# Kernel tuning notes

Hardware: AMD Instinct MI355X
Metric: run time of the kernel (lower is better)

Reference implementation:

```python
import math
import jax
import jax.numpy as jnp
import numpy as np
from jax import lax

B, L, D = 4, 1024, 512
NL = 2           # encoder layers
E, K = 8, 4      # num_experts, top_k (SparseMoE defaults)
H = 4 * D        # expert hidden
NOISE_KEY = jax.random.key(42)


def _layer_norm(x, g, b, eps=1e-5):
    m = jnp.mean(x, axis=-1, keepdims=True)
    v = jnp.mean((x - m) ** 2, axis=-1, keepdims=True)
    return (x - m) * lax.rsqrt(v + eps) * g + b


def setup_inputs() -> dict:
    key = jax.random.key(0)
    ks = iter(jax.random.split(key, 64))
    s = 0.02

    def nrm(shape):
        return jax.random.normal(next(ks), shape, dtype=jnp.float32) * s

    inp = {
        "x": jax.random.normal(next(ks), (B, L, D), dtype=jnp.float32),
        "norm_coord": jax.random.uniform(next(ks), (B, L, 2), dtype=jnp.float32),
        "mask": jnp.triu(jnp.ones((L, L), dtype=bool), k=1),           # causal
        "src_key_padding_mask": jnp.zeros((B, L), dtype=bool),
        # per-layer stacked params (leading dim NL)
        "wq": nrm((NL, D, D)), "bq": jnp.zeros((NL, D)),
        "wk": nrm((NL, D, D)), "bk": jnp.zeros((NL, D)),
        "wv": nrm((NL, D, D)), "bv": jnp.zeros((NL, D)),
        "wr": nrm((NL, 2, D // 2)),                                    # RoPE freq proj (no bias)
        "ln1_g": jnp.ones((NL, D)), "ln1_b": jnp.zeros((NL, D)),
        "rt_w": nrm((NL, D, E)), "rt_b": jnp.zeros((NL, E)),           # router
        "nz_w": nrm((NL, D, E)), "nz_b": jnp.zeros((NL, E)),           # noise
        "ew1": nrm((NL, E, D, H)), "eb1": jnp.zeros((NL, E, H)),
        "ew2": nrm((NL, E, H, D)), "eb2": jnp.zeros((NL, E, D)),
        "ln2_g": jnp.ones((NL, D)), "ln2_b": jnp.zeros((NL, D)),
    }
    return inp


def _encoder(x, norm_coord, mask, src_key_padding_mask,
             wq, bq, wk, bk, wv, bv, wr, ln1_g, ln1_b,
             rt_w, rt_b, nz_w, nz_b, ew1, eb1, ew2, eb2, ln2_g, ln2_b):
    neg = jnp.float32(-jnp.inf)
    attn_mask = mask[None, :, :] | src_key_padding_mask[:, None, :]  # [B,L,L]
    for l in range(NL):
        # ---- RoPE attention ----
        q = x @ wq[l] + bq[l]
        k = x @ wk[l] + bk[l]
        v = x @ wv[l] + bv[l]
        f = norm_coord @ wr[l]                    # [B,L,D/2] angles
        cosf, sinf = jnp.cos(f), jnp.sin(f)

        def rot(t):
            t2 = t.reshape(B, L, D // 2, 2)
            re = t2[..., 0] * cosf - t2[..., 1] * sinf
            im = t2[..., 0] * sinf + t2[..., 1] * cosf
            return jnp.stack([re, im], axis=-1).reshape(B, L, D)

        q, k = rot(q), rot(k)
        scores = jnp.einsum("bqd,bkd->bqk", q, k) / math.sqrt(D)
        scores = jnp.where(attn_mask, neg, scores)
        attn = jax.nn.softmax(scores, axis=-1)
        x = x + jnp.einsum("bqk,bkd->bqd", attn, v)
        x = _layer_norm(x, ln1_g[l], ln1_b[l])

        # ---- noisy top-k MoE ----
        logits = x @ rt_w[l] + rt_b[l]            # [B,L,E]
        noise_logits = x @ nz_w[l] + nz_b[l]
        eps = jax.random.normal(jax.random.fold_in(NOISE_KEY, l), logits.shape, dtype=logits.dtype)
        noisy = logits + eps * jax.nn.softplus(noise_logits)
        top_v, top_i = lax.top_k(noisy, K)        # [B,L,K]
        sel = jax.nn.one_hot(top_i, E, dtype=noisy.dtype).sum(axis=-2) > 0  # [B,L,E]
        gate = jax.nn.softmax(jnp.where(sel, noisy, neg), axis=-1)          # zero on non-topk
        moe = jnp.zeros_like(x)
        for e in range(E):  # gate is exactly 0 for non-selected experts => same math as masked dispatch
            h = jax.nn.relu(x @ ew1[l, e] + eb1[l, e])
            moe = moe + (h @ ew2[l, e] + eb2[l, e]) * gate[..., e:e + 1]
        x = _layer_norm(x + moe, ln2_g[l], ln2_b[l])
    return x


def reference(x, norm_coord, mask, src_key_padding_mask,
              wq, bq, wk, bk, wv, bv, wr, ln1_g, ln1_b,
              rt_w, rt_b, nz_w, nz_b, ew1, eb1, ew2, eb2, ln2_g, ln2_b):
    return _encoder(x, norm_coord, mask, src_key_padding_mask,
                    wq, bq, wk, bk, wv, bv, wr, ln1_g, ln1_b,
                    rt_w, rt_b, nz_w, nz_b, ew1, eb1, ew2, eb2, ln2_g, ln2_b)
```

## Files before the change

### kernel.cpp

```cpp
#include <hip/hip_runtime.h>
#include <math.h>

#define TOK 4096
#define DMODEL 512
#define LSEQ 1024
#define BATCH 4
#define NLAYER 2
#define NEXP 8
#define TOPK 4
#define HDIM 2048
#define NBLK 136
#define CHBLK 68
#define KSPLIT2 4

typedef unsigned short u16;
typedef __attribute__((ext_vector_type(8))) short bf16x8;
typedef __attribute__((ext_vector_type(4))) float f32x4;

__device__ __forceinline__ u16 f2bf(float x) {
  const unsigned u = __float_as_uint(x);
  return (u16)((u + 0x7FFFu + ((u >> 16) & 1u)) >> 16);
}
__device__ __forceinline__ float bf2f(u16 h) {
  return __uint_as_float(((unsigned)h) << 16);
}

__device__ __forceinline__ float waveAllSum(float v) {
#pragma unroll
  for (int off = 1; off < 64; off <<= 1) v += __shfl_xor(v, off, 64);
  return v;
}
__device__ __forceinline__ float waveAllMax(float v) {
#pragma unroll
  for (int off = 1; off < 64; off <<= 1) v = fmaxf(v, __shfl_xor(v, off, 64));
  return v;
}

__device__ __forceinline__ unsigned rotl32(unsigned x, int r) {
  return (x << r) | (x >> (32 - r));
}
__device__ __forceinline__ void tf2x32(unsigned k0, unsigned k1,
                                       unsigned& x0, unsigned& x1) {
  const unsigned ks0 = k0, ks1 = k1, ks2 = k0 ^ k1 ^ 0x1BD11BDAu;
  x0 += ks0; x1 += ks1;
#define TF_R4(a, b, c, d)                                   \
  x0 += x1; x1 = rotl32(x1, a); x1 ^= x0;                   \
  x0 += x1; x1 = rotl32(x1, b); x1 ^= x0;                   \
  x0 += x1; x1 = rotl32(x1, c); x1 ^= x0;                   \
  x0 += x1; x1 = rotl32(x1, d); x1 ^= x0;
  TF_R4(13, 15, 26, 6)  x0 += ks1; x1 += ks2 + 1u;
  TF_R4(17, 29, 16, 24) x0 += ks2; x1 += ks0 + 2u;
  TF_R4(13, 15, 26, 6)  x0 += ks0; x1 += ks1 + 3u;
  TF_R4(17, 29, 16, 24) x0 += ks1; x1 += ks2 + 4u;
  TF_R4(13, 15, 26, 6)  x0 += ks2; x1 += ks0 + 5u;
#undef TF_R4
}

__device__ __forceinline__ float xla_erfinv(float u) {
  float w = -log1pf(-__fmul_rn(u, u));
  float p;
  if (w < 5.0f) {
    w = __fadd_rn(w, -2.5f);
    p = 2.81022636e-08f;
    p = __fadd_rn(3.43273939e-07f, __fmul_rn(p, w));
    p = __fadd_rn(-3.5233877e-06f, __fmul_rn(p, w));
    p = __fadd_rn(-4.39150654e-06f, __fmul_rn(p, w));
    p = __fadd_rn(0.00021858087f, __fmul_rn(p, w));
    p = __fadd_rn(-0.00125372503f, __fmul_rn(p, w));
    p = __fadd_rn(-0.00417768164f, __fmul_rn(p, w));
    p = __fadd_rn(0.246640727f, __fmul_rn(p, w));
    p = __fadd_rn(1.50140941f, __fmul_rn(p, w));
  } else {
    w = __fadd_rn(sqrtf(w), -3.0f);
    p = -0.000200214257f;
    p = __fadd_rn(0.000100950558f, __fmul_rn(p, w));
    p = __fadd_rn(0.00134934322f, __fmul_rn(p, w));
    p = __fadd_rn(-0.00367342844f, __fmul_rn(p, w));
    p = __fadd_rn(0.00573950773f, __fmul_rn(p, w));
    p = __fadd_rn(-0.0076224613f, __fmul_rn(p, w));
    p = __fadd_rn(0.00943887047f, __fmul_rn(p, w));
    p = __fadd_rn(1.00167406f, __fmul_rn(p, w));
    p = __fadd_rn(2.83297682f, __fmul_rn(p, w));
  }
  return __fmul_rn(p, u);
}

__device__ __forceinline__ float bits_to_normal(unsigned bits) {
  const unsigned fb = (bits >> 9) | 0x3f800000u;
  const float u01 = __fadd_rn(__uint_as_float(fb), -1.0f);
  const float lo = -0.99999994f;
  float u = __fadd_rn(__fmul_rn(u01, 2.0f), lo);
  u = fmaxf(u, lo);
  return __fmul_rn(1.41421356237309515f, xla_erfinv(u));
}

__device__ __forceinline__ float eps_normal(unsigned i, unsigned layer) {
  unsigned f0 = 0u, f1 = layer;
  tf2x32(0u, 42u, f0, f1);
  unsigned x0 = 0u, x1 = i;
  tf2x32(f0, f1, x0, x1);
  return bits_to_normal(x0 ^ x1);
}

__global__ __launch_bounds__(256) void split_f32_bf16(
    const float* __restrict__ in, u16* __restrict__ hi, u16* __restrict__ lo,
    int n) {
  const int i = (blockIdx.x * 256 + threadIdx.x) * 4;
  if (i >= n) return;
  const float4 v = *(const float4*)(in + i);
  ushort4 h, l;
  h.x = f2bf(v.x); l.x = f2bf(v.x - bf2f(h.x));
  h.y = f2bf(v.y); l.y = f2bf(v.y - bf2f(h.y));
  h.z = f2bf(v.z); l.z = f2bf(v.z - bf2f(h.z));
  h.w = f2bf(v.w); l.w = f2bf(v.w - bf2f(h.w));
  *(ushort4*)(hi + i) = h;
  *(ushort4*)(lo + i) = l;
}

__global__ __launch_bounds__(256) void transpose_split(
    const float* __restrict__ in, u16* __restrict__ hi, u16* __restrict__ lo,
    int R, int C) {
  __shared__ float tile[32][33];
  const size_t eoff = (size_t)blockIdx.z * R * C;
  const float* src = in + eoff;
  const int r0 = blockIdx.y * 32, c0 = blockIdx.x * 32;
  const int tx = threadIdx.x & 31, ty = threadIdx.x >> 5;
#pragma unroll
  for (int j = 0; j < 4; ++j)
    tile[ty + 8 * j][tx] = src[(size_t)(r0 + ty + 8 * j) * C + c0 + tx];
  __syncthreads();
  u16* dh = hi + eoff;
  u16* dl = lo + eoff;
#pragma unroll
  for (int j = 0; j < 4; ++j) {
    const float v = tile[tx][ty + 8 * j];
    const u16 h = f2bf(v);
    const size_t idx = (size_t)(c0 + ty + 8 * j) * R + r0 + tx;
    dh[idx] = h;
    dl[idx] = f2bf(v - bf2f(h));
  }
}

#define SWZC(lane) ((((lane) >> 4) ^ ((lane) & 3)) * 8)

template <int PASSES>
__global__ __launch_bounds__(256) void mfma_gemm3(
    const u16* __restrict__ Ahi, const u16* __restrict__ Alo,
    const u16* __restrict__ Bhi, const u16* __restrict__ Blo,
    const float* __restrict__ bias, float* __restrict__ Cg,
    int N, int K, float alpha,
    long long sA, long long sB, long long sC) {
  constexpr int NT = 128 * 40;
  __shared__ u16 lds[(PASSES == 3 ? 4 : 2) * NT];
  u16(*As)[40] = (u16(*)[40])lds;
  u16(*Bs)[40] = (u16(*)[40])(lds + NT);
  u16(*Als)[40] = (u16(*)[40])(lds + 2 * NT);
  u16(*Bls)[40] = (u16(*)[40])(lds + 3 * NT);
  const int m0 = blockIdx.y * 128, n0 = blockIdx.x * 128;
  const int t = threadIdx.x;
  const int sr = t >> 1, c0 = (t & 1) * 2;
  const int w0 = ((c0) ^ (sr & 3)) * 8, w1 = ((c0 + 1) ^ (sr & 3)) * 8;
  const u16* aH = Ahi + (long long)blockIdx.z * sA + (size_t)(m0 + sr) * K;
  const u16* aL = Alo + (long long)blockIdx.z * sA + (size_t)(m0 + sr) * K;
  const u16* bH = Bhi + (long long)blockIdx.z * sB + (size_t)(n0 + sr) * K;
  const u16* bL = Blo + (long long)blockIdx.z * sB + (size_t)(n0 + sr) * K;
  float* C = Cg + (long long)blockIdx.z * sC;
  const int lane = t & 63, w = t >> 6;
  const int wm = (w >> 1) * 64, wn = (w & 1) * 64;
  const int lr = lane & 15;
  const int kcol = SWZC(lane);

  f32x4 acc[4][4] = {};
  for (int k0 = 0; k0 < K; k0 += 32) {
    __syncthreads();
    *(uint4*)&As[sr][w0] = *(const uint4*)(aH + k0 + c0 * 8);
    *(uint4*)&As[sr][w1] = *(const uint4*)(aH + k0 + c0 * 8 + 8);
    *(uint4*)&Bs[sr][w0] = *(const uint4*)(bH + k0 + c0 * 8);
    *(uint4*)&Bs[sr][w1] = *(const uint4*)(bH + k0 + c0 * 8 + 8);
    if constexpr (PASSES == 3) {
      *(uint4*)&Als[sr][w0] = *(const uint4*)(aL + k0 + c0 * 8);
      *(uint4*)&Als[sr][w1] = *(const uint4*)(aL + k0 + c0 * 8 + 8);
      *(uint4*)&Bls[sr][w0] = *(const uint4*)(bL + k0 + c0 * 8);
      *(uint4*)&Bls[sr][w1] = *(const uint4*)(bL + k0 + c0 * 8 + 8);
    }
    __syncthreads();
    bf16x8 ah[4], bh[4];
#pragma unroll
    for (int i = 0; i < 4; ++i) {
      ah[i] = *(const bf16x8*)&As[wm + i * 16 + lr][kcol];
      bh[i] = *(const bf16x8*)&Bs[wn + i * 16 + lr][kcol];
    }
    if constexpr (PASSES == 3) {
      bf16x8 al[4], bl[4];
#pragma unroll
      for (int i = 0; i < 4; ++i) {
        al[i] = *(const bf16x8*)&Als[wm + i * 16 + lr][kcol];
        bl[i] = *(const bf16x8*)&Bls[wn + i * 16 + lr][kcol];
      }
#pragma unroll
      for (int i = 0; i < 4; ++i)
#pragma unroll
        for (int j = 0; j < 4; ++j) {
          acc[i][j] = __builtin_amdgcn_mfma_f32_16x16x32_bf16(ah[i], bh[j], acc[i][j], 0, 0, 0);
          acc[i][j] = __builtin_amdgcn_mfma_f32_16x16x32_bf16(al[i], bh[j], acc[i][j], 0, 0, 0);
          acc[i][j] = __builtin_amdgcn_mfma_f32_16x16x32_bf16(ah[i], bl[j], acc[i][j], 0, 0, 0);
        }
    } else {
#pragma unroll
      for (int i = 0; i < 4; ++i)
#pragma unroll
        for (int j = 0; j < 4; ++j)
          acc[i][j] = __builtin_amdgcn_mfma_f32_16x16x32_bf16(ah[i], bh[j], acc[i][j], 0, 0, 0);
    }
  }
#pragma unroll
  for (int i = 0; i < 4; ++i) {
#pragma unroll
    for (int j = 0; j < 4; ++j) {
      const int n = n0 + wn + j * 16 + lr;
      const float bv = bias ? bias[n] : 0.f;
#pragma unroll
      for (int r = 0; r < 4; ++r) {
        const int m = m0 + wm + i * 16 + (lane >> 4) * 4 + r;
        C[(size_t)m * N + n] = acc[i][j][r] * alpha + bv;
      }
    }
  }
}

__global__ __launch_bounds__(256) void mfma_qkv3(
    const u16* __restrict__ Ahi, const u16* __restrict__ Alo,
    const u16* __restrict__ Wq_h, const u16* __restrict__ Wq_l,
    const u16* __restrict__ Wk_h, const u16* __restrict__ Wk_l,
    const u16* __restrict__ Wv_h, const u16* __restrict__ Wv_l,
    const float* __restrict__ bq, const float* __restrict__ bk,
    const float* __restrict__ bv,
    float* __restrict__ qo, float* __restrict__ ko, float* __restrict__ vo) {
  constexpr int K = DMODEL;
  constexpr int NT = 128 * 40;
  __shared__ u16 lds[4 * NT];
  u16(*As)[40] = (u16(*)[40])lds;
  u16(*Bs)[40] = (u16(*)[40])(lds + NT);
  u16(*Als)[40] = (u16(*)[40])(lds + 2 * NT);
  u16(*Bls)[40] = (u16(*)[40])(lds + 3 * NT);
  const int mat = blockIdx.x >> 2;
  const u16* Bhi = (mat == 0) ? Wq_h : (mat == 1) ? Wk_h : Wv_h;
  const u16* Blo = (mat == 0) ? Wq_l : (mat == 1) ? Wk_l : Wv_l;
  const float* bias = (mat == 0) ? bq : (mat == 1) ? bk : bv;
  float* C = (mat == 0) ? qo : (mat == 1) ? ko : vo;
  const int m0 = blockIdx.y * 128, n0 = (blockIdx.x & 3) * 128;
  const int t = threadIdx.x;
  const int sr = t >> 1, c0 = (t & 1) * 2;
  const int w0 = ((c0) ^ (sr & 3)) * 8, w1 = ((c0 + 1) ^ (sr & 3)) * 8;
  const u16* aH = Ahi + (size_t)(m0 + sr) * K;
  const u16* aL = Alo + (size_t)(m0 + sr) * K;
  const u16* bH = Bhi + (size_t)(n0 + sr) * K;
  const u16* bL = Blo + (size_t)(n0 + sr) * K;
  const int lane = t & 63, w = t >> 6;
  const int wm = (w >> 1) * 64, wn = (w & 1) * 64;
  const int lr = lane & 15;
  const int kcol = SWZC(lane);

  f32x4 acc[4][4] = {};
  for (int k0 = 0; k0 < K; k0 += 32) {
    __syncthreads();
    *(uint4*)&As[sr][w0] = *(const uint4*)(aH + k0 + c0 * 8);
    *(uint4*)&As[sr][w1] = *(const uint4*)(aH + k0 + c0 * 8 + 8);
    *(uint4*)&Bs[sr][w0] = *(const uint4*)(bH + k0 + c0 * 8);
    *(uint4*)&Bs[sr][w1] = *(const uint4*)(bH + k0 + c0 * 8 + 8);
    *(uint4*)&Als[sr][w0] = *(const uint4*)(aL + k0 + c0 * 8);
    *(uint4*)&Als[sr][w1] = *(const uint4*)(aL + k0 + c0 * 8 + 8);
    *(uint4*)&Bls[sr][w0] = *(const uint4*)(bL + k0 + c0 * 8);
    *(uint4*)&Bls[sr][w1] = *(const uint4*)(bL + k0 + c0 * 8 + 8);
    __syncthreads();
    bf16x8 ah[4], bh[4], al[4], bl[4];
#pragma unroll
    for (int i = 0; i < 4; ++i) {
      ah[i] = *(const bf16x8*)&As[wm + i * 16 + lr][kcol];
      bh[i] = *(const bf16x8*)&Bs[wn + i * 16 + lr][kcol];
      al[i] = *(const bf16x8*)&Als[wm + i * 16 + lr][kcol];
      bl[i] = *(const bf16x8*)&Bls[wn + i * 16 + lr][kcol];
    }
#pragma unroll
    for (int i = 0; i < 4; ++i)
#pragma unroll
      for (int j = 0; j < 4; ++j) {
        acc[i][j] = __builtin_amdgcn_mfma_f32_16x16x32_bf16(ah[i], bh[j], acc[i][j], 0, 0, 0);
        acc[i][j] = __builtin_amdgcn_mfma_f32_16x16x32_bf16(al[i], bh[j], acc[i][j], 0, 0, 0);
        acc[i][j] = __builtin_amdgcn_mfma_f32_16x16x32_bf16(ah[i], bl[j], acc[i][j], 0, 0, 0);
      }
  }
#pragma unroll
  for (int i = 0; i < 4; ++i) {
#pragma unroll
    for (int j = 0; j < 4; ++j) {
      const int n = n0 + wn + j * 16 + lr;
      const float bv2 = bias[n];
#pragma unroll
      for (int r = 0; r < 4; ++r) {
        const int m = m0 + wm + i * 16 + (lane >> 4) * 4 + r;
        C[(size_t)m * DMODEL + n] = acc[i][j][r] + bv2;
      }
    }
  }
}

template <int PASSES>
__global__ __launch_bounds__(256) void mfma_moe1(
    const u16* __restrict__ Ahi, const u16* __restrict__ Alo,
    const u16* __restrict__ Bhi, const u16* __restrict__ Blo,
    const float* __restrict__ b1l, const int* __restrict__ list,
    const int* __restrict__ blockExp, const int* __restrict__ blockBase,
    const int* __restrict__ blockValid, int byOff,
    u16* __restrict__ Hhi, u16* __restrict__ Hlo) {
  constexpr int K = DMODEL;
  constexpr int NT = 128 * 40;
  __shared__ u16 lds[(PASSES == 3 ? 4 : 2) * NT];
  u16(*As)[40] = (u16(*)[40])lds;
  u16(*Bs)[40] = (u16(*)[40])(lds + NT);
  u16(*Als)[40] = (u16(*)[40])(lds + 2 * NT);
  u16(*Bls)[40] = (u16(*)[40])(lds + 3 * NT);
  const int by = byOff + blockIdx.y;
  const int e = blockExp[by];
  if (e < 0) return;
  const int row0 = blockBase[by], valid = blockValid[by];
  const int hbase = blockBase[byOff];
  const int n0 = blockIdx.x * 128;
  const int t = threadIdx.x;
  const int sr = t >> 1, c0 = (t & 1) * 2;
  const int w0 = ((c0) ^ (sr & 3)) * 8, w1 = ((c0 + 1) ^ (sr & 3)) * 8;
  const int atok = list[row0 + ((sr < valid) ? sr : 0)];
  const u16* aH = Ahi + (size_t)atok * K;
  const u16* aL = Alo + (size_t)atok * K;
  const u16* bH = Bhi + ((size_t)e * HDIM + n0 + sr) * K;
  const u16* bL = Blo + ((size_t)e * HDIM + n0 + sr) * K;
  const int lane = t & 63, w = t >> 6;
  const int wm = (w >> 1) * 64, wn = (w & 1) * 64;
  const int lr = lane & 15;
  const int kcol = SWZC(lane);

  f32x4 acc[4][4] = {};
  for (int k0 = 0; k0 < K; k0 += 32) {
    __syncthreads();
    *(uint4*)&As[sr][w0] = *(const uint4*)(aH + k0 + c0 * 8);
    *(uint4*)&As[sr][w1] = *(const uint4*)(aH + k0 + c0 * 8 + 8);
    *(uint4*)&Bs[sr][w0] = *(const uint4*)(bH + k0 + c0 * 8);
    *(uint4*)&Bs[sr][w1] = *(const uint4*)(bH + k0 + c0 * 8 + 8);
    if constexpr (PASSES == 3) {
      *(uint4*)&Als[sr][w0] = *(const uint4*)(aL + k0 + c0 * 8);
      *(uint4*)&Als[sr][w1] = *(const uint4*)(aL + k0 + c0 * 8 + 8);
      *(uint4*)&Bls[sr][w0] = *(const uint4*)(bL + k0 + c0 * 8);
      *(uint4*)&Bls[sr][w1] = *(const uint4*)(bL + k0 + c0 * 8 + 8);
    }
    __syncthreads();
    bf16x8 ah[4], bh[4];
#pragma unroll
    for (int i = 0; i < 4; ++i) {
      ah[i] = *(const bf16x8*)&As[wm + i * 16 + lr][kcol];
      bh[i] = *(const bf16x8*)&Bs[wn + i * 16 + lr][kcol];
    }
    if constexpr (PASSES == 3) {
      bf16x8 al[4], bl[4];
#pragma unroll
      for (int i = 0; i < 4; ++i) {
        al[i] = *(const bf16x8*)&Als[wm + i * 16 + lr][kcol];
        bl[i] = *(const bf16x8*)&Bls[wn + i * 16 + lr][kcol];
      }
#pragma unroll
      for (int i = 0; i < 4; ++i)
#pragma unroll
        for (int j = 0; j < 4; ++j) {
          acc[i][j] = __builtin_amdgcn_mfma_f32_16x16x32_bf16(ah[i], bh[j], acc[i][j], 0, 0, 0);
          acc[i][j] = __builtin_amdgcn_mfma_f32_16x16x32_bf16(al[i], bh[j], acc[i][j], 0, 0, 0);
          acc[i][j] = __builtin_amdgcn_mfma_f32_16x16x32_bf16(ah[i], bl[j], acc[i][j], 0, 0, 0);
        }
    } else {
#pragma unroll
      for (int i = 0; i < 4; ++i)
#pragma unroll
        for (int j = 0; j < 4; ++j)
          acc[i][j] = __builtin_amdgcn_mfma_f32_16x16x32_bf16(ah[i], bh[j], acc[i][j], 0, 0, 0);
    }
  }
#pragma unroll
  for (int i = 0; i < 4; ++i) {
#pragma unroll
    for (int j = 0; j < 4; ++j) {
      const int n = n0 + wn + j * 16 + lr;
      const float bv = b1l[(size_t)e * HDIM + n];
#pragma unroll
      for (int r = 0; r < 4; ++r) {
        const int m = wm + i * 16 + (lane >> 4) * 4 + r;
        if (m < valid) {
          const float h = fmaxf(acc[i][j][r] + bv, 0.f);
          const u16 hh = f2bf(h);
          const size_t idx = (size_t)(row0 + m - hbase) * HDIM + n;
          Hhi[idx] = hh;
          if constexpr (PASSES == 3) Hlo[idx] = f2bf(h - bf2f(hh));
        }
      }
    }
  }
}

template <int PASSES>
__global__ __launch_bounds__(256) void mfma_moe2(
    const u16* __restrict__ Hhi, const u16* __restrict__ Hlo,
    const u16* __restrict__ Bhi, const u16* __restrict__ Blo,
    const float* __restrict__ b2l, const int* __restrict__ list,
    const int* __restrict__ blockExp, const int* __restrict__ blockBase,
    const int* __restrict__ blockValid, int byOff,
    const float* __restrict__ rowGate, float* __restrict__ moe) {
  constexpr int K = HDIM;
  constexpr int KC = K / KSPLIT2;
  constexpr int NT = 128 * 40;
  __shared__ u16 lds[(PASSES == 3 ? 4 : 2) * NT];
  u16(*As)[40] = (u16(*)[40])lds;
  u16(*Bs)[40] = (u16(*)[40])(lds + NT);
  u16(*Als)[40] = (u16(*)[40])(lds + 2 * NT);
  u16(*Bls)[40] = (u16(*)[40])(lds + 3 * NT);
  const int by = byOff + blockIdx.y;
  const int e = blockExp[by];
  if (e < 0) return;
  const int row0 = blockBase[by], valid = blockValid[by];
  const int hbase = blockBase[byOff];
  const int n0 = blockIdx.x * 128;
  const int kb = blockIdx.z * KC;
  const int t = threadIdx.x;
  const int sr = t >> 1, c0 = (t & 1) * 2;
  const int w0 = ((c0) ^ (sr & 3)) * 8, w1 = ((c0 + 1) ^ (sr & 3)) * 8;
  const u16* aH = Hhi + (size_t)(row0 + sr - hbase) * K;
  const u16* aL = Hlo + (size_t)(row0 + sr - hbase) * K;
  const u16* bH = Bhi + ((size_t)e * DMODEL + n0 + sr) * K;
  const u16* bL = Blo + ((size_t)e * DMODEL + n0 + sr) * K;
  const int lane = t & 63, w = t >> 6;
  const int wm = (w >> 1) * 64, wn = (w & 1) * 64;
  const int lr = lane & 15;
  const int kcol = SWZC(lane);

  f32x4 acc[4][4] = {};
  for (int k0 = kb; k0 < kb + KC; k0 += 32) {
    __syncthreads();
    *(uint4*)&As[sr][w0] = *(const uint4*)(aH + k0 + c0 * 8);
    *(uint4*)&As[sr][w1] = *(const uint4*)(aH + k0 + c0 * 8 + 8);
    *(uint4*)&Bs[sr][w0] = *(const uint4*)(bH + k0 + c0 * 8);
    *(uint4*)&Bs[sr][w1] = *(const uint4*)(bH + k0 + c0 * 8 + 8);
    if constexpr (PASSES == 3) {
      *(uint4*)&Als[sr][w0] = *(const uint4*)(aL + k0 + c0 * 8);
      *(uint4*)&Als[sr][w1] = *(const uint4*)(aL + k0 + c0 * 8 + 8);
      *(uint4*)&Bls[sr][w0] = *(const uint4*)(bL + k0 + c0 * 8);
      *(uint4*)&Bls[sr][w1] = *(const uint4*)(bL + k0 + c0 * 8 + 8);
    }
    __syncthreads();
    bf16x8 ah[4], bh[4];
#pragma unroll
    for (int i = 0; i < 4; ++i) {
      ah[i] = *(const bf16x8*)&As[wm + i * 16 + lr][kcol];
      bh[i] = *(const bf16x8*)&Bs[wn + i * 16 + lr][kcol];
    }
    if constexpr (PASSES == 3) {
      bf16x8 al[4], bl[4];
#pragma unroll
      for (int i = 0; i < 4; ++i) {
        al[i] = *(const bf16x8*)&Als[wm + i * 16 + lr][kcol];
        bl[i] = *(const bf16x8*)&Bls[wn + i * 16 + lr][kcol];
      }
#pragma unroll
      for (int i = 0; i < 4; ++i)
#pragma unroll
        for (int j = 0; j < 4; ++j) {
          acc[i][j] = __builtin_amdgcn_mfma_f32_16x16x32_bf16(ah[i], bh[j], acc[i][j], 0, 0, 0);
          acc[i][j] = __builtin_amdgcn_mfma_f32_16x16x32_bf16(al[i], bh[j], acc[i][j], 0, 0, 0);
          acc[i][j] = __builtin_amdgcn_mfma_f32_16x16x32_bf16(ah[i], bl[j], acc[i][j], 0, 0, 0);
        }
    } else {
#pragma unroll
      for (int i = 0; i < 4; ++i)
#pragma unroll
        for (int j = 0; j < 4; ++j)
          acc[i][j] = __builtin_amdgcn_mfma_f32_16x16x32_bf16(ah[i], bh[j], acc[i][j], 0, 0, 0);
    }
  }
  const bool addBias = (blockIdx.z == 0);
#pragma unroll
  for (int i = 0; i < 4; ++i) {
#pragma unroll
    for (int r = 0; r < 4; ++r) {
      const int m = wm + i * 16 + (lane >> 4) * 4 + r;
      if (m >= valid) continue;
      const int tok = list[row0 + m];
      const float g = rowGate[row0 + m];
      float* orow = moe + (size_t)tok * DMODEL;
#pragma unroll
      for (int j = 0; j < 4; ++j) {
        const int n = n0 + wn + j * 16 + lr;
        float v = acc[i][j][r];
        if (addBias) v += b2l[(size_t)e * DMODEL + n];
        atomicAdd(orow + n, v * g);
      }
    }
  }
}

__global__ __launch_bounds__(256) void rope_rot(
    float* __restrict__ q, float* __restrict__ k,
    const float* __restrict__ nc, const float* __restrict__ wr) {
  const int tok = blockIdx.x, j = threadIdx.x;
  const float c0 = nc[tok * 2 + 0], c1 = nc[tok * 2 + 1];
  const float f = c0 * wr[j] + c1 * wr[256 + j];
  const float cf = cosf(f), sf = sinf(f);
  float2* q2 = (float2*)(q + (long long)tok * DMODEL);
  float2* k2 = (float2*)(k + (long long)tok * DMODEL);
  const float2 qq = q2[j];
  const float2 kk = k2[j];
  q2[j] = make_float2(qq.x * cf - qq.y * sf, qq.x * sf + qq.y * cf);
  k2[j] = make_float2(kk.x * cf - kk.y * sf, kk.x * sf + kk.y * cf);
}

__global__ __launch_bounds__(256) void attn_softmax(
    float* __restrict__ S, const unsigned char* __restrict__ pad) {
  const int q = blockIdx.x & (LSEQ - 1);
  const int b = blockIdx.x >> 10;
  float* row = S + (long long)blockIdx.x * LSEQ;
  const int t = threadIdx.x;
  const float4 v = ((const float4*)row)[t];
  float vals[4] = {v.x, v.y, v.z, v.w};
  const int k0 = t * 4;
#pragma unroll
  for (int j = 0; j < 4; ++j) {
    const int k = k0 + j;
    if (k > q || pad[b * LSEQ + k]) vals[j] = -INFINITY;
  }
  __shared__ float red[4];
  const int wid = t >> 6, lane = t & 63;
  float m = waveAllMax(fmaxf(fmaxf(vals[0], vals[1]), fmaxf(vals[2], vals[3])));
  if (lane == 0) red[wid] = m;
  __syncthreads();
  m = fmaxf(fmaxf(red[0], red[1]), fmaxf(red[2], red[3]));
  const float e0 = expf(vals[0] - m), e1 = expf(vals[1] - m);
  const float e2 = expf(vals[2] - m), e3 = expf(vals[3] - m);
  const float ps = waveAllSum(e0 + e1 + e2 + e3);
  __syncthreads();
  if (lane == 0) red[wid] = ps;
  __syncthreads();
  const float tot = red[0] + red[1] + red[2] + red[3];
  float4 o;
  o.x = e0 / tot; o.y = e1 / tot; o.z = e2 / tot; o.w = e3 / tot;
  ((float4*)row)[t] = o;
}

__global__ __launch_bounds__(128) void ln_add(
    const float* __restrict__ Aa, const float* __restrict__ Bb,
    const float* __restrict__ gg, const float* __restrict__ bb,
    float* __restrict__ out) {
  const int row = blockIdx.x, t = threadIdx.x;
  const float4 va = ((const float4*)(Aa + (long long)row * DMODEL))[t];
  const float4 vb = ((const float4*)(Bb + (long long)row * DMODEL))[t];
  const float x0 = va.x + vb.x, x1 = va.y + vb.y;
  const float x2 = va.z + vb.z, x3 = va.w + vb.w;
  __shared__ float r1[2], r2[2];
  const int wid = t >> 6, lane = t & 63;
  const float s = waveAllSum(x0 + x1 + x2 + x3);
  if (lane == 0) r1[wid] = s;
  __syncthreads();
  const float mean = (r1[0] + r1[1]) * (1.0f / DMODEL);
  const float d0 = x0 - mean, d1 = x1 - mean, d2 = x2 - mean, d3 = x3 - mean;
  const float vs = waveAllSum(d0 * d0 + d1 * d1 + d2 * d2 + d3 * d3);
  if (lane == 0) r2[wid] = vs;
  __syncthreads();
  const float var = (r2[0] + r2[1]) * (1.0f / DMODEL);
  const float rs = rsqrtf(var + 1e-5f);
  const float4 g4 = ((const float4*)gg)[t];
  const float4 b4 = ((const float4*)bb)[t];
  float4 o;
  o.x = d0 * rs * g4.x + b4.x;
  o.y = d1 * rs * g4.y + b4.y;
  o.z = d2 * rs * g4.z + b4.z;
  o.w = d3 * rs * g4.w + b4.w;
  ((float4*)(out + (long long)row * DMODEL))[t] = o;
}

__global__ __launch_bounds__(256) void router_topk2(
    const float* __restrict__ x, const float* __restrict__ rtw,
    const float* __restrict__ rtb, const float* __restrict__ nzw,
    const float* __restrict__ nzb, float* __restrict__ gate,
    int* __restrict__ counts, unsigned char* __restrict__ selmask, int layer) {
  __shared__ float Wl[16][524];
  __shared__ float noisyS[16][8];
  const int t = threadIdx.x;
  for (int i = t; i < DMODEL * NEXP; i += 256) {
    const int d = i >> 3, e = i & 7;
    Wl[e][d] = rtw[i];
    Wl[8 + e][d] = nzw[i];
  }
  __syncthreads();
  const int tt = t >> 4, o = t & 15;
  const int tok = blockIdx.x * 16 + tt;
  const float4* x4 = (const float4*)(x + (size_t)tok * DMODEL);
  float s = 0.f;
#pragma unroll 4
  for (int dd = 0; dd < DMODEL / 4; ++dd) {
    const float4 xv = x4[dd];
    const float4 wv = *(const float4*)&Wl[o][dd * 4];
    s = fmaf(xv.x, wv.x, s);
    s = fmaf(xv.y, wv.y, s);
    s = fmaf(xv.z, wv.z, s);
    s = fmaf(xv.w, wv.w, s);
  }
  const float other = __shfl_xor(s, 8, 64);
  if (o < 8) {
    const float logit = s + rtb[o];
    const float nl = other + nzb[o];
    const float eps = eps_normal((unsigned)(tok * NEXP + o), (unsigned)layer);
    const float sp = fmaxf(nl, 0.f) + log1pf(expf(-fabsf(nl)));
    noisyS[tt][o] = logit + eps * sp;
  }
  __syncthreads();
  if (t < 16) {
    const int tk = blockIdx.x * 16 + t;
    float v[8]; bool sel[8];
#pragma unroll
    for (int i = 0; i < 8; ++i) { v[i] = noisyS[t][i]; sel[i] = false; }
    for (int r = 0; r < TOPK; ++r) {
      int bi = 0; float best = -INFINITY;
      for (int i = 0; i < 8; ++i)
        if (!sel[i] && v[i] > best) { best = v[i]; bi = i; }
      sel[bi] = true;
    }
    float m = -INFINITY;
    for (int i = 0; i < 8; ++i) if (sel[i]) m = fmaxf(m, v[i]);
    float ex[8]; float den = 0.f;
    unsigned char mbits = 0;
    for (int i = 0; i < 8; ++i) {
      ex[i] = sel[i] ? expf(v[i] - m) : 0.f;
      den += ex[i];
      if (sel[i]) { mbits |= (unsigned char)(1u << i); atomicAdd(&counts[i], 1); }
    }
    for (int i = 0; i < 8; ++i) gate[tk * NEXP + i] = ex[i] / den;
    selmask[tk] = mbits;
  }
}

__global__ void moe_plan(const int* __restrict__ counts, int* __restrict__ start,
                         int* __restrict__ blockExp, int* __restrict__ blockBase,
                         int* __restrict__ blockValid) {
  if (threadIdx.x != 0) return;
  int s = 0, by = 0;
  for (int e = 0; e < NEXP; ++e) {
    start[e] = s;
    const int c = counts[e];
    const int nb = (c + 127) >> 7;
    for (int b = 0; b < nb; ++b) {
      blockExp[by] = e;
      blockBase[by] = s + b * 128;
      blockValid[by] = min(128, c - b * 128);
      ++by;
    }
    s += nb * 128;
  }
  for (; by < NBLK; ++by) { blockExp[by] = -1; blockBase[by] = s; blockValid[by] = 0; }
}

__global__ __launch_bounds__(256) void moe_build(
    const unsigned char* __restrict__ selmask, const int* __restrict__ start,
    int* __restrict__ cursor, int* __restrict__ list,
    const float* __restrict__ gate, float* __restrict__ rowGate) {
  const int tok = blockIdx.x * 256 + threadIdx.x;
  if (tok >= TOK) return;
  unsigned m = selmask[tok];
  while (m) {
    const int e = __ffs(m) - 1;
    m &= m - 1;
    const int slot = atomicAdd(&cursor[e], 1);
    list[start[e] + slot] = tok;
    rowGate[start[e] + slot] = gate[tok * NEXP + e];
  }
}

__global__ __launch_bounds__(256) void zero_f32(float* __restrict__ p, int n4) {
  const int i = blockIdx.x * 256 + threadIdx.x;
  if (i < n4) ((float4*)p)[i] = make_float4(0.f, 0.f, 0.f, 0.f);
}
__global__ void zero_i32(int* __restrict__ p, int n) {
  const int i = threadIdx.x;
  if (i < n) p[i] = 0;
}

extern "C" void kernel_launch(void* const* d_in, const int* in_sizes, int n_in,
                              void* d_out, int out_size, void* d_ws,
                              size_t ws_size, hipStream_t stream) {
  const float* x_in = (const float*)d_in[0];
  const float* nc = (const float*)d_in[1];
  const unsigned char* pad = (const unsigned char*)d_in[3];
  const float* wq = (const float*)d_in[4];
  const float* bq = (const float*)d_in[5];
  const float* wk = (const float*)d_in[6];
  const float* bk = (const float*)d_in[7];
  const float* wv = (const float*)d_in[8];
  const float* bv = (const float*)d_in[9];
  const float* wr = (const float*)d_in[10];
  const float* ln1g = (const float*)d_in[11];
  const float* ln1b = (const float*)d_in[12];
  const float* rtw = (const float*)d_in[13];
  const float* rtb = (const float*)d_in[14];
  const float* nzw = (const float*)d_in[15];
  const float* nzb = (const float*)d_in[16];
  const float* ew1 = (const float*)d_in[17];
  const float* eb1 = (const float*)d_in[18];
  const float* ew2 = (const float*)d_in[19];
  const float* eb2 = (const float*)d_in[20];
  const float* ln2g = (const float*)d_in[21];
  const float* ln2b = (const float*)d_in[22];

  float* ws = (float*)d_ws;
  const long long SZ = (long long)TOK * DMODEL;
  float* qb = ws;
  float* kb = ws + SZ;
  float* vb2 = ws + 2 * SZ;
  float* xcur = ws + 3 * SZ;
  float* moe = ws + 4 * SZ;
  float* gate = ws + 5 * SZ;
  int* meta = (int*)(ws + 10518528);
  int* counts = meta;
  int* cursor = meta + 8;
  int* startE = meta + 16;
  int* blockExp = meta + 24;
  int* blockBase = meta + 160;
  int* blockValid = meta + 296;
  int* list = meta + 432;
  unsigned char* selmask = (unsigned char*)(meta + 17840);
  float* rowGate = ws + 10537408;
  u16* Xhi = (u16*)(ws + 10554816);
  u16* Xlo = (u16*)(ws + 11603392);

  float* scores = ws + 12651968;
  u16* ub = (u16*)(ws + 16846272);
  u16* XAhi = ub;
  u16* XAlo = ub + 2097152;
  u16* Qhi = ub + 4194304;
  u16* Qlo = ub + 6291456;
  u16* Khi = ub + 8388608;
  u16* Klo = ub + 10485760;
  u16* Phi = ub + 12582912;
  u16* Plo = ub + 16777216;
  u16* VThi = ub + 20971520;
  u16* VTlo = ub + 23068672;
  u16* WqThi = ub + 25165824;
  u16* WqTlo = ub + 25427968;
  u16* WkThi = ub + 25690112;
  u16* WkTlo = ub + 25952256;
  u16* WvThi = ub + 26214400;
  u16* WvTlo = ub + 26476544;

  u16* W1Thi = (u16*)(ws + 12651968);
  u16* W1Tlo = (u16*)(ws + 16846272);
  u16* W2Thi = (u16*)(ws + 21040576);
  u16* W2Tlo = (u16*)(ws + 25234880);
  u16* Hhi = (u16*)(ws + 29429184);
  u16* Hlo = (u16*)(ws + 38342080);

  const float iscale = 1.0f / sqrtf((float)DMODEL);
  const dim3 blk(256);
  const long long sQ = (long long)LSEQ * DMODEL;
  const long long sS = (long long)LSEQ * LSEQ;

  for (int l = 0; l < NLAYER; ++l) {
    const float* xl = (l == 0) ? x_in : xcur;
    const long long wOff = (long long)l * DMODEL * DMODEL;

    split_f32_bf16<<<2048, blk, 0, stream>>>(xl, XAhi, XAlo, (int)SZ);
    transpose_split<<<dim3(16, 16, 1), blk, 0, stream>>>(wq + wOff, WqThi, WqTlo, DMODEL, DMODEL);
    transpose_split<<<dim3(16, 16, 1), blk, 0, stream>>>(wk + wOff, WkThi, WkTlo, DMODEL, DMODEL);
    transpose_split<<<dim3(16, 16, 1), blk, 0, stream>>>(wv + wOff, WvThi, WvTlo, DMODEL, DMODEL);
    mfma_qkv3<<<dim3(12, TOK / 128), blk, 0, stream>>>(
        XAhi, XAlo, WqThi, WqTlo, WkThi, WkTlo, WvThi, WvTlo,
        bq + l * DMODEL, bk + l * DMODEL, bv + l * DMODEL, qb, kb, vb2);

    rope_rot<<<TOK, 256, 0, stream>>>(qb, kb, nc, wr + (long long)l * DMODEL);

    split_f32_bf16<<<2048, blk, 0, stream>>>(qb, Qhi, Qlo, (int)SZ);
    split_f32_bf16<<<2048, blk, 0, stream>>>(kb, Khi, Klo, (int)SZ);
    mfma_gemm3<3><<<dim3(8, 8, BATCH), blk, 0, stream>>>(
        Qhi, Qlo, Khi, Klo, nullptr, scores, LSEQ, DMODEL, iscale, sQ, sQ, sS);

    attn_softmax<<<BATCH * LSEQ, 256, 0, stream>>>(scores, pad);

    split_f32_bf16<<<4096, blk, 0, stream>>>(scores, Phi, Plo, (int)(4 * sS / 4 * 4));
    transpose_split<<<dim3(16, 32, BATCH), blk, 0, stream>>>(vb2, VThi, VTlo, LSEQ, DMODEL);
    mfma_gemm3<3><<<dim3(4, 8, BATCH), blk, 0, stream>>>(
        Phi, Plo, VThi, VTlo, nullptr, qb, DMODEL, LSEQ, 1.f, sS, sQ, sQ);

    ln_add<<<TOK, 128, 0, stream>>>(xl, qb, ln1g + l * DMODEL, ln1b + l * DMODEL, xcur);

    zero_i32<<<1, 64, 0, stream>>>(counts, 16);
    router_topk2<<<TOK / 16, blk, 0, stream>>>(
        xcur, rtw + l * DMODEL * NEXP, rtb + l * NEXP, nzw + l * DMODEL * NEXP,
        nzb + l * NEXP, gate, counts, selmask, l);
    moe_plan<<<1, 64, 0, stream>>>(counts, startE, blockExp, blockBase, blockValid);
    moe_build<<<TOK / 256, 256, 0, stream>>>(selmask, startE, cursor, list, gate, rowGate);
    zero_f32<<<(int)(SZ / 4 / 256), 256, 0, stream>>>(moe, (int)(SZ / 4));

    split_f32_bf16<<<2048, blk, 0, stream>>>(xcur, Xhi, Xlo, (int)SZ);
    transpose_split<<<dim3(64, 16, 8), blk, 0, stream>>>(
        ew1 + (long long)l * NEXP * DMODEL * HDIM, W1Thi, W1Tlo, DMODEL, HDIM);
    transpose_split<<<dim3(16, 64, 8), blk, 0, stream>>>(
        ew2 + (long long)l * NEXP * HDIM * DMODEL, W2Thi, W2Tlo, HDIM, DMODEL);

    const float* b1l = eb1 + (long long)l * NEXP * HDIM;
    const float* b2l = eb2 + (long long)l * NEXP * DMODEL;
    for (int ch = 0; ch < 2; ++ch) {
      const int byOff = ch * CHBLK;
      mfma_moe1<3><<<dim3(HDIM / 128, CHBLK), blk, 0, stream>>>(
          Xhi, Xlo, W1Thi, W1Tlo, b1l, list, blockExp, blockBase, blockValid,
          byOff, Hhi, Hlo);
      mfma_moe2<3><<<dim3(DMODEL / 128, CHBLK, KSPLIT2), blk, 0, stream>>>(
          Hhi, Hlo, W2Thi, W2Tlo, b2l, list, blockExp, blockBase, blockValid,
          byOff, rowGate, moe);
    }

    float* outp = (l == NLAYER - 1) ? (float*)d_out : xcur;
    ln_add<<<TOK, 128, 0, stream>>>(xcur, moe, ln2g + l * DMODEL, ln2b + l * DMODEL, outp);
  }
}
```

Baseline: 1.708 ms.

## Replace atomic MoE dispatch with deterministic ballot-based count, scan, and fill

Drops the global atomic counters used for per-expert token counts and slot assignment. Per-block expert counts are now computed with wave ballots, a single-thread kernel scans them into per-block offsets, and a fill kernel places each token in its expert list by ballot prefix. This removes atomic contention and the zero_i32 launch, and makes list order deterministic, at the cost of one extra small kernel launch and a serial scan.

Result: faster. 1.408 ms (-17.6%).

```diff
diff --git a/kernel.cpp b/kernel.cpp
--- a/kernel.cpp
+++ b/kernel.cpp
@@ -584,7 +584,7 @@
     const float* __restrict__ x, const float* __restrict__ rtw,
     const float* __restrict__ rtb, const float* __restrict__ nzw,
     const float* __restrict__ nzb, float* __restrict__ gate,
-    int* __restrict__ counts, unsigned char* __restrict__ selmask, int layer) {
+    unsigned char* __restrict__ selmask, int layer) {
   __shared__ float Wl[16][524];
   __shared__ float noisyS[16][8];
   const int t = threadIdx.x;
@@ -634,26 +634,48 @@
     for (int i = 0; i < 8; ++i) {
       ex[i] = sel[i] ? expf(v[i] - m) : 0.f;
       den += ex[i];
-      if (sel[i]) { mbits |= (unsigned char)(1u << i); atomicAdd(&counts[i], 1); }
+      if (sel[i]) mbits |= (unsigned char)(1u << i);
     }
     for (int i = 0; i < 8; ++i) gate[tk * NEXP + i] = ex[i] / den;
     selmask[tk] = mbits;
   }
 }
 
-__global__ void moe_plan(const int* __restrict__ counts, int* __restrict__ start,
-                         int* __restrict__ blockExp, int* __restrict__ blockBase,
-                         int* __restrict__ blockValid) {
+__global__ __launch_bounds__(256) void moe_count(
+    const unsigned char* __restrict__ selmask, int* __restrict__ blockCnt) {
+  __shared__ int wcnt[4][8];
+  const int t = threadIdx.x, lane = t & 63, w = t >> 6;
+  const unsigned m = selmask[blockIdx.x * 256 + t];
+#pragma unroll
+  for (int e = 0; e < 8; ++e) {
+    const unsigned long long bal = __ballot((m >> e) & 1u);
+    if (lane == 0) wcnt[w][e] = __popcll(bal);
+  }
+  __syncthreads();
+  if (t < 8)
+    blockCnt[blockIdx.x * 8 + t] =
+        wcnt[0][t] + wcnt[1][t] + wcnt[2][t] + wcnt[3][t];
+}
+
+__global__ void moe_scan(const int* __restrict__ blockCnt,
+                         int* __restrict__ start, int* __restrict__ blockExp,
+                         int* __restrict__ blockBase, int* __restrict__ blockValid,
+                         int* __restrict__ blockOff) {
   if (threadIdx.x != 0) return;
   int s = 0, by = 0;
   for (int e = 0; e < NEXP; ++e) {
     start[e] = s;
-    const int c = counts[e];
+    int off = s;
+    for (int b = 0; b < TOK / 256; ++b) {
+      blockOff[b * 8 + e] = off;
+      off += blockCnt[b * 8 + e];
+    }
+    const int c = off - s;
     const int nb = (c + 127) >> 7;
-    for (int b = 0; b < nb; ++b) {
+    for (int b2 = 0; b2 < nb; ++b2) {
       blockExp[by] = e;
-      blockBase[by] = s + b * 128;
-      blockValid[by] = min(128, c - b * 128);
+      blockBase[by] = s + b2 * 128;
+      blockValid[by] = min(128, c - b2 * 128);
       ++by;
     }
     s += nb * 128;
@@ -661,29 +683,44 @@
   for (; by < NBLK; ++by) { blockExp[by] = -1; blockBase[by] = s; blockValid[by] = 0; }
 }
 
-__global__ __launch_bounds__(256) void moe_build(
-    const unsigned char* __restrict__ selmask, const int* __restrict__ start,
-    int* __restrict__ cursor, int* __restrict__ list,
-    const float* __restrict__ gate, float* __restrict__ rowGate) {
-  const int tok = blockIdx.x * 256 + threadIdx.x;
-  if (tok >= TOK) return;
-  unsigned m = selmask[tok];
-  while (m) {
-    const int e = __ffs(m) - 1;
-    m &= m - 1;
-    const int slot = atomicAdd(&cursor[e], 1);
-    list[start[e] + slot] = tok;
-    rowGate[start[e] + slot] = gate[tok * NEXP + e];
+__global__ __launch_bounds__(256) void moe_fill(
+    const unsigned char* __restrict__ selmask, const int* __restrict__ blockOff,
+    const float* __restrict__ gate, int* __restrict__ list,
+    float* __restrict__ rowGate) {
+  __shared__ int wbase[4][8];
+  const int t = threadIdx.x, lane = t & 63, w = t >> 6;
+  const int tok = blockIdx.x * 256 + t;
+  const unsigned m = selmask[tok];
+  unsigned long long bal[8];
+#pragma unroll
+  for (int e = 0; e < 8; ++e) {
+    bal[e] = __ballot((m >> e) & 1u);
+    if (lane == 0) wbase[w][e] = __popcll(bal[e]);
+  }
+  __syncthreads();
+  if (t < 8) {
+    int base = blockOff[blockIdx.x * 8 + t];
+    for (int ww = 0; ww < 4; ++ww) {
+      const int c = wbase[ww][t];
+      wbase[ww][t] = base;
+      base += c;
+    }
+  }
+  __syncthreads();
+  const unsigned long long ltm = (1ull << lane) - 1ull;
+#pragma unroll
+  for (int e = 0; e < 8; ++e) {
+    if ((m >> e) & 1u) {
+      const int slot = wbase[w][e] + __popcll(bal[e] & ltm);
+      list[slot] = tok;
+      rowGate[slot] = gate[tok * NEXP + e];
+    }
   }
 }
 
 __global__ __launch_bounds__(256) void zero_f32(float* __restrict__ p, int n4) {
   const int i = blockIdx.x * 256 + threadIdx.x;
   if (i < n4) ((float4*)p)[i] = make_float4(0.f, 0.f, 0.f, 0.f);
-}
-__global__ void zero_i32(int* __restrict__ p, int n) {
-  const int i = threadIdx.x;
-  if (i < n) p[i] = 0;
 }
 
 extern "C" void kernel_launch(void* const* d_in, const int* in_sizes, int n_in,
@@ -721,8 +758,6 @@
   float* moe = ws + 4 * SZ;
   float* gate = ws + 5 * SZ;
   int* meta = (int*)(ws + 10518528);
-  int* counts = meta;
-  int* cursor = meta + 8;
   int* startE = meta + 16;
   int* blockExp = meta + 24;
   int* blockBase = meta + 160;
@@ -758,6 +793,8 @@
   u16* W2Tlo = (u16*)(ws + 25234880);
   u16* Hhi = (u16*)(ws + 29429184);
   u16* Hlo = (u16*)(ws + 38342080);
+  int* blockCnt = (int*)(ws + 47254976);
+  int* blockOff = (int*)(ws + 47255104);
 
   const float iscale = 1.0f / sqrtf((float)DMODEL);
   const dim3 blk(256);
@@ -792,12 +829,13 @@
 
     ln_add<<<TOK, 128, 0, stream>>>(xl, qb, ln1g + l * DMODEL, ln1b + l * DMODEL, xcur);
 
-    zero_i32<<<1, 64, 0, stream>>>(counts, 16);
     router_topk2<<<TOK / 16, blk, 0, stream>>>(
         xcur, rtw + l * DMODEL * NEXP, rtb + l * NEXP, nzw + l * DMODEL * NEXP,
-        nzb + l * NEXP, gate, counts, selmask, l);
-    moe_plan<<<1, 64, 0, stream>>>(counts, startE, blockExp, blockBase, blockValid);
-    moe_build<<<TOK / 256, 256, 0, stream>>>(selmask, startE, cursor, list, gate, rowGate);
+        nzb + l * NEXP, gate, selmask, l);
+    moe_count<<<TOK / 256, blk, 0, stream>>>(selmask, blockCnt);
+    moe_scan<<<1, 64, 0, stream>>>(blockCnt, startE, blockExp, blockBase,
+                                   blockValid, blockOff);
+    moe_fill<<<TOK / 256, blk, 0, stream>>>(selmask, blockOff, gate, list, rowGate);
     zero_f32<<<(int)(SZ / 4 / 256), 256, 0, stream>>>(moe, (int)(SZ / 4));
 
     split_f32_bf16<<<2048, blk, 0, stream>>>(xcur, Xhi, Xlo, (int)SZ);
```
